# Kernel optimization log

Hardware: AMD Instinct MI355X
Metric: run time of the kernel (lower is better)

The kernel has to match this reference:

```python
import jax, jax.numpy as jnp
import numpy as np
from jax import lax

DN = ('NHWC', 'HWIO', 'NHWC')
EPS = 1e-3  # keras BatchNormalization default epsilon


def conv2d(x, w):
    return lax.conv_general_dilated(x, w, (1, 1), 'SAME', dimension_numbers=DN)


def convlstm2d(x, W, U, b):
    # x: (B,T,H,Wd,Cin); W: (kh,kw,Cin,4F); U: (kh,kw,F,4F); b: (4F,)
    # Keras ConvLSTM2D, gate order i,f,c,o; recurrent_activation=sigmoid, activation=relu
    B, T, H, Wd, _ = x.shape
    F = U.shape[2]
    xz = conv2d(x.reshape(B * T, H, Wd, -1), W).reshape(B, T, H, Wd, 4 * F) + b

    def step(carry, xt):
        h, c = carry
        z = xt + conv2d(h, U)
        i, f, g, o = jnp.split(z, 4, axis=-1)
        i = jax.nn.sigmoid(i)
        f = jax.nn.sigmoid(f)
        c = f * c + i * jax.nn.relu(g)
        h = jax.nn.sigmoid(o) * jax.nn.relu(c)
        return (h, c), h

    h0 = jnp.zeros((B, H, Wd, F), x.dtype)
    _, hs = lax.scan(step, (h0, h0), jnp.moveaxis(xz, 0, 1))  # (T,B,H,W,F)
    return jnp.moveaxis(hs, 0, 1)


def batchnorm(x, gamma, beta, mean, var):
    return (x - mean) * (gamma * lax.rsqrt(var + EPS)) + beta


def maxpool_122(x):
    # MaxPooling3D pool=(1,2,2), strides=(1,2,2), padding='same', channels_last
    return lax.reduce_window(x, -jnp.inf, lax.max, (1, 1, 2, 2, 1), (1, 1, 2, 2, 1), 'SAME')


def setup_inputs() -> dict:
    key = jax.random.key(0)
    ks = iter(jax.random.split(key, 32))
    s = 0.05
    d = {
        'x': jax.random.normal(next(ks), (8, 10, 64, 64, 3), jnp.float32),
        'W1': jax.random.normal(next(ks), (5, 5, 3, 128), jnp.float32) * s,
        'U1': jax.random.normal(next(ks), (5, 5, 32, 128), jnp.float32) * s,
        'b1': jnp.zeros((128,), jnp.float32),
        'g1': jax.random.uniform(next(ks), (32,), jnp.float32, 0.5, 1.5),
        'be1': jax.random.normal(next(ks), (32,), jnp.float32) * 0.1,
        'm1': jax.random.normal(next(ks), (32,), jnp.float32) * 0.1,
        'v1': jax.random.uniform(next(ks), (32,), jnp.float32, 0.5, 1.5),
        'W2': jax.random.normal(next(ks), (5, 5, 32, 128), jnp.float32) * s,
        'U2': jax.random.normal(next(ks), (5, 5, 32, 128), jnp.float32) * s,
        'b2': jnp.zeros((128,), jnp.float32),
        'g2': jax.random.uniform(next(ks), (32,), jnp.float32, 0.5, 1.5),
        'be2': jax.random.normal(next(ks), (32,), jnp.float32) * 0.1,
        'm2': jax.random.normal(next(ks), (32,), jnp.float32) * 0.1,
        'v2': jax.random.uniform(next(ks), (32,), jnp.float32, 0.5, 1.5),
        'W3': jax.random.normal(next(ks), (3, 3, 32, 128), jnp.float32) * s,
        'U3': jax.random.normal(next(ks), (3, 3, 32, 128), jnp.float32) * s,
        'b3': jnp.zeros((128,), jnp.float32),
        'g3': jax.random.uniform(next(ks), (32,), jnp.float32, 0.5, 1.5),
        'be3': jax.random.normal(next(ks), (32,), jnp.float32) * 0.1,
        'm3': jax.random.normal(next(ks), (32,), jnp.float32) * 0.1,
        'v3': jax.random.uniform(next(ks), (32,), jnp.float32, 0.5, 1.5),
        'Wd1': jax.random.normal(next(ks), (20480, 64), jnp.float32) * 0.01,
        'bd1': jnp.zeros((64,), jnp.float32),
        'Wd2': jax.random.normal(next(ks), (64, 10), jnp.float32) * 0.1,
        'bd2': jnp.zeros((10,), jnp.float32),
    }
    return d


def reference(x, W1, U1, b1, g1, be1, m1, v1, W2, U2, b2, g2, be2, m2, v2,
              W3, U3, b3, g3, be3, m3, v3, Wd1, bd1, Wd2, bd2):
    x = convlstm2d(x, W1, U1, b1)
    x = maxpool_122(batchnorm(x, g1, be1, m1, v1))
    x = convlstm2d(x, W2, U2, b2)
    x = maxpool_122(batchnorm(x, g2, be2, m2, v2))
    x = convlstm2d(x, W3, U3, b3)
    x = maxpool_122(batchnorm(x, g3, be3, m3, v3))
    x = x.reshape(x.shape[0], -1)  # (B, T*H*W*F) = (8, 20480)
    x = jax.nn.softmax(x @ Wd1 + bd1, axis=-1)
    return jax.nn.softmax(x @ Wd2 + bd2, axis=-1)
```

## Files before the change

### kernel.cpp

```cpp
#include <hip/hip_runtime.h>

using short8 = __attribute__((ext_vector_type(8))) short;
using f32x4  = __attribute__((ext_vector_type(4))) float;

__device__ __forceinline__ unsigned short f2bf(float x){
    unsigned u = __float_as_uint(x);
    unsigned r = (u + 0x7FFFu + ((u>>16)&1u)) >> 16;
    return (unsigned short)r;
}
__device__ __forceinline__ float bf2f(unsigned short h){
    return __uint_as_float(((unsigned)h)<<16);
}
__device__ __forceinline__ float sigf(float x){ return 1.0f/(1.0f+__expf(-x)); }
__device__ __forceinline__ int swz(int b){ return b ^ (((b>>7)&7)<<4); }

struct SP {
    const float *x;
    const float *g1,*be1,*m1,*v1;
    const float *g2,*be2,*m2,*v2;
    const float *g3,*be3,*m3,*v3;
    unsigned short *hs1,*hs2,*hs3;
    unsigned short *pl1,*pl2,*pl3;
    float *cst1,*cst2,*cst3;
    const short8 *U1b,*W1b,*U2b,*W2b,*U3b,*W3b;
    const float *bp;
    unsigned *ctr;
};

__global__ __launch_bounds__(256)
void xform_all(const float* __restrict__ U1, const float* __restrict__ W1,
               const float* __restrict__ U2, const float* __restrict__ W2,
               const float* __restrict__ U3, const float* __restrict__ W3,
               const float* __restrict__ b1, const float* __restrict__ b2, const float* __restrict__ b3,
               short8* __restrict__ U1b, short8* __restrict__ W1b,
               short8* __restrict__ U2b, short8* __restrict__ W2b,
               short8* __restrict__ U3b, short8* __restrict__ W3b,
               float* __restrict__ bp)
{
    int i = blockIdx.x*256 + threadIdx.x;
    if (i >= 49536) return;
    if (i >= 49152) {
        int j = i - 49152, layer = j >> 7, np = j & 127;
        int oc = ((np>>4)&3)*32 + (np>>6)*16 + (np&15);
        const float* bs = layer==0 ? b1 : (layer==1 ? b2 : b3);
        bp[j] = bs[oc];
        return;
    }
    const float* src; short8* dst; int base, kmax;
    if      (i < 12800){ src=U1; dst=U1b; base=0;     kmax=800; }
    else if (i < 14336){ src=W1; dst=W1b; base=12800; kmax=75;  }
    else if (i < 27136){ src=U2; dst=U2b; base=14336; kmax=800; }
    else if (i < 39936){ src=W2; dst=W2b; base=27136; kmax=800; }
    else if (i < 44544){ src=U3; dst=U3b; base=39936; kmax=288; }
    else               { src=W3; dst=W3b; base=44544; kmax=288; }
    int j = i - base;
    int lane = j & 63, nt = (j >> 6) & 7, tap = j >> 9;
    int np = nt*16 + (lane & 15);
    int oc = ((np>>4)&3)*32 + (np>>6)*16 + (np&15);
    int g = lane >> 4;
    short8 pk;
    #pragma unroll
    for (int e = 0; e < 8; ++e) {
        int k = tap*32 + g*8 + e;
        unsigned short v = (k < kmax) ? f2bf(src[(long)k*128 + oc]) : (unsigned short)0;
        pk[e] = (short)v;
    }
    dst[j] = pk;
}

template<int K, int PW, int MT2>
__device__ __forceinline__ void conv_taps(f32x4 (&acc)[MT2][4],
    const unsigned short* patch, const short8* Wf, int mh, int nh, int l15, int g4, int lane)
{
    constexpr int NTAP = K*K;
    const short8* ub = Wf + nh*4*64 + lane;
    short8 bA0 = ub[0], bA1 = ub[64], bA2 = ub[128], bA3 = ub[192];
    short8 bB0 = bA0, bB1 = bA1, bB2 = bA2, bB3 = bA3;
    { const short8* u = ub + 512; bB0=u[0]; bB1=u[64]; bB2=u[128]; bB3=u[192]; }
    #pragma unroll 1
    for (int tp = 0; tp < NTAP; tp += 2) {
        {
            int dy = tp / K, dx = tp % K;
            #pragma unroll
            for (int mt = 0; mt < MT2; ++mt) {
                short8 af = *(const short8*)((const char*)patch +
                    swz(((mh*MT2 + mt + dy)*PW + l15 + dx)*64 + g4*16));
                acc[mt][0] = __builtin_amdgcn_mfma_f32_16x16x32_bf16(af, bA0, acc[mt][0], 0,0,0);
                acc[mt][1] = __builtin_amdgcn_mfma_f32_16x16x32_bf16(af, bA1, acc[mt][1], 0,0,0);
                acc[mt][2] = __builtin_amdgcn_mfma_f32_16x16x32_bf16(af, bA2, acc[mt][2], 0,0,0);
                acc[mt][3] = __builtin_amdgcn_mfma_f32_16x16x32_bf16(af, bA3, acc[mt][3], 0,0,0);
            }
            if (tp + 2 < NTAP) { const short8* u = ub + (long)(tp+2)*512; bA0=u[0];bA1=u[64];bA2=u[128];bA3=u[192]; }
        }
        if (tp + 1 < NTAP) {
            int dy = (tp+1) / K, dx = (tp+1) % K;
            #pragma unroll
            for (int mt = 0; mt < MT2; ++mt) {
                short8 af = *(const short8*)((const char*)patch +
                    swz(((mh*MT2 + mt + dy)*PW + l15 + dx)*64 + g4*16));
                acc[mt][0] = __builtin_amdgcn_mfma_f32_16x16x32_bf16(af, bB0, acc[mt][0], 0,0,0);
                acc[mt][1] = __builtin_amdgcn_mfma_f32_16x16x32_bf16(af, bB1, acc[mt][1], 0,0,0);
                acc[mt][2] = __builtin_amdgcn_mfma_f32_16x16x32_bf16(af, bB2, acc[mt][2], 0,0,0);
                acc[mt][3] = __builtin_amdgcn_mfma_f32_16x16x32_bf16(af, bB3, acc[mt][3], 0,0,0);
            }
            if (tp + 3 < NTAP) { const short8* u = ub + (long)(tp+3)*512; bB0=u[0];bB1=u[64];bB2=u[128];bB3=u[192]; }
        }
    }
}

template<int MT2>
__device__ __forceinline__ void lstm_epilogue(
    f32x4 (&acc)[MT2][4], unsigned short* hs, float* cst, unsigned short* plout,
    const float* gg, const float* bb, const float* mm, const float* vv,
    int H, int W, int n, int y0, int x0, int t, int mh, int nh, int l15, int g4, int first)
{
    const int f = nh*16 + l15;
    const int xt = x0 >> 4;
    const float sc = gg[f] * rsqrtf(vv[f] + 1e-3f);
    const float sh = bb[f] - mm[f]*sc;
    unsigned short* outh = hs + ((long)n*10 + t)*(long)H*W*32;
    float hv[MT2][4];
    #pragma unroll
    for (int mt = 0; mt < MT2; ++mt) {
        int row = y0 + mh*MT2 + mt;
        long tb = ((long)(n*H + row)*(W>>4) + xt)*512 + f*16 + g4*4;
        f32x4 cold = first ? (f32x4){0.f,0.f,0.f,0.f} : *(const f32x4*)&cst[tb];
        f32x4 cn;
        #pragma unroll
        for (int j = 0; j < 4; ++j) {
            float zi = acc[mt][0][j];
            float zf = acc[mt][1][j];
            float zg = acc[mt][2][j];
            float zo = acc[mt][3][j];
            float c2 = sigf(zf)*cold[j] + sigf(zi)*fmaxf(zg, 0.0f);
            cn[j] = c2;
            float h = sigf(zo)*fmaxf(c2, 0.0f);
            hv[mt][j] = h;
            outh[((long)row*W + (x0 + g4*4 + j))*32 + f] = f2bf(h);
        }
        *(f32x4*)&cst[tb] = cn;
    }
    #pragma unroll
    for (int mp = 0; mp < MT2/2; ++mp) {
        int orow = (y0>>1) + mh*(MT2/2) + mp;
        #pragma unroll
        for (int jp = 0; jp < 2; ++jp) {
            int ocol = (x0>>1) + g4*2 + jp;
            float mx = fmaxf(fmaxf(hv[2*mp][2*jp],   hv[2*mp][2*jp+1]),
                             fmaxf(hv[2*mp+1][2*jp], hv[2*mp+1][2*jp+1]));
            plout[(((long)(n*10 + t)*(H>>1) + orow)*(W>>1) + ocol)*32 + f] = f2bf(mx*sc + sh);
        }
    }
}

__device__ void l1_step(char* smem, const SP& p, int n, int y0, int x0, int t)
{
    constexpr int PAD = 2, PH = 12, PW = 20, MT2 = 4, MPX = 128;
    const int H = 64, W = 64;
    unsigned short* patch_s = (unsigned short*)smem;
    unsigned short* xpk_s   = (unsigned short*)(smem + 15360);
    unsigned short* xraw    = (unsigned short*)(smem + 39936);
    const int tid = threadIdx.x;
    const int lane = tid & 63, wid = tid >> 6;
    const int mh = wid >> 1, nh = wid & 1;
    const int l15 = lane & 15, g4 = lane >> 4;
    const int first = (t == 0);

    short8 z8 = {0,0,0,0,0,0,0,0};
    #pragma unroll
    for (int c = tid; c < MPX*96/8; c += 256)
        ((short8*)xpk_s)[c] = z8;

    if (tid < PH*PW) {
        const float* xs = p.x + ((long)n*10 + t)*4096*3;
        int gy = y0 - PAD + tid / PW;
        int gx = x0 - PAD + tid % PW;
        float v0=0.f, v1=0.f, v2=0.f;
        if ((unsigned)gy < 64u && (unsigned)gx < 64u) {
            const float* b = xs + ((long)gy*64 + gx)*3;
            v0 = b[0]; v1 = b[1]; v2 = b[2];
        }
        xraw[tid*3]   = f2bf(v0);
        xraw[tid*3+1] = f2bf(v1);
        xraw[tid*3+2] = f2bf(v2);
    }

    if (!first) {
        const unsigned short* s = p.hs1 + ((long)n*10 + (t-1))*(long)H*W*32;
        #pragma unroll 1
        for (int c = tid; c < PH*PW*4; c += 256) {
            int pix = c >> 2, gq = c & 3;
            int pr = pix / PW, pc = pix % PW;
            int gy = y0 - PAD + pr, gx = x0 - PAD + pc;
            short8 v = z8;
            if ((unsigned)gy < 64u && (unsigned)gx < 64u)
                v = *(const short8*)(s + ((long)gy*W + gx)*32 + gq*8);
            *(short8*)((char*)patch_s + swz(pix*64 + gq*16)) = v;
        }
    }
    __syncthreads();

    #pragma unroll 1
    for (int c = tid; c < MPX*25; c += 256) {
        int px = c & (MPX-1), tap = c >> 7;
        int dy = (tap*52) >> 8, dx = tap - dy*5;
        int pi = ((px>>4) + dy)*PW + (px&15) + dx;
        int o = px*192 + tap*6;
        *(unsigned short*)((char*)xpk_s + swz(o))   = xraw[pi*3];
        *(unsigned short*)((char*)xpk_s + swz(o+2)) = xraw[pi*3+1];
        *(unsigned short*)((char*)xpk_s + swz(o+4)) = xraw[pi*3+2];
    }
    __syncthreads();

    f32x4 acc[MT2][4];
    #pragma unroll
    for (int ntl = 0; ntl < 4; ++ntl) {
        float bv = p.bp[(nh*4+ntl)*16 + l15];
        #pragma unroll
        for (int mt = 0; mt < MT2; ++mt)
            acc[mt][ntl] = (f32x4){bv,bv,bv,bv};
    }
    #pragma unroll 1
    for (int c = 0; c < 3; ++c) {
        const short8* wp = p.W1b + ((long)c*8 + nh*4)*64 + lane;
        short8 bf0 = wp[0], bf1 = wp[64], bf2 = wp[128], bf3 = wp[192];
        #pragma unroll
        for (int mt = 0; mt < MT2; ++mt) {
            short8 af = *(const short8*)((const char*)xpk_s +
                swz(((mh*MT2+mt)*16 + l15)*192 + c*64 + g4*16));
            acc[mt][0] = __builtin_amdgcn_mfma_f32_16x16x32_bf16(af, bf0, acc[mt][0], 0,0,0);
            acc[mt][1] = __builtin_amdgcn_mfma_f32_16x16x32_bf16(af, bf1, acc[mt][1], 0,0,0);
            acc[mt][2] = __builtin_amdgcn_mfma_f32_16x16x32_bf16(af, bf2, acc[mt][2], 0,0,0);
            acc[mt][3] = __builtin_amdgcn_mfma_f32_16x16x32_bf16(af, bf3, acc[mt][3], 0,0,0);
        }
    }
    if (!first)
        conv_taps<5,PW,MT2>(acc, patch_s, p.U1b, mh, nh, l15, g4, lane);

    lstm_epilogue<MT2>(acc, p.hs1, p.cst1, p.pl1, p.g1, p.be1, p.m1, p.v1,
                       H, W, n, y0, x0, t, mh, nh, l15, g4, first);
}

template<int K, int HH>
__device__ void l23_step(char* smem, const SP& p,
    unsigned short* hs, const unsigned short* plin, unsigned short* plout, float* cst,
    const short8* Ufr, const short8* Wfr, const float* bp,
    const float* gg, const float* bb, const float* mm, const float* vv,
    int n, int y0, int x0, int t)
{
    constexpr int TH = 4, PAD = K/2, PH = TH+K-1, PW = 16+K-1, MT2 = 2;
    const int H = HH, W = HH;
    unsigned short* patchH = (unsigned short*)smem;
    unsigned short* patchX = (unsigned short*)(smem + PH*PW*64);

    const int tid = threadIdx.x;
    const int lane = tid & 63, wid = tid >> 6;
    const int mh = wid >> 1, nh = wid & 1;
    const int l15 = lane & 15, g4 = lane >> 4;
    const int first = (t == 0);

    const unsigned short* hsrc = hs + ((long)n*10 + (t-1))*(long)H*W*32;
    const unsigned short* xsrc = plin + ((long)n*10 + t)*(long)H*W*32;
    short8 z8 = {0,0,0,0,0,0,0,0};
    #pragma unroll 1
    for (int c = tid; c < PH*PW*4; c += 256) {
        int pix = c >> 2, gq = c & 3;
        int pr = pix / PW, pc = pix % PW;
        int gy = y0 - PAD + pr, gx = x0 - PAD + pc;
        short8 vx = z8, vh = z8;
        if ((unsigned)gy < (unsigned)H && (unsigned)gx < (unsigned)W) {
            vx = *(const short8*)(xsrc + ((long)gy*W + gx)*32 + gq*8);
            if (!first) vh = *(const short8*)(hsrc + ((long)gy*W + gx)*32 + gq*8);
        }
        *(short8*)((char*)patchX + swz(pix*64 + gq*16)) = vx;
        *(short8*)((char*)patchH + swz(pix*64 + gq*16)) = vh;
    }
    __syncthreads();

    f32x4 acc[MT2][4];
    #pragma unroll
    for (int ntl = 0; ntl < 4; ++ntl) {
        float bv = bp[(nh*4+ntl)*16 + l15];
        #pragma unroll
        for (int mt = 0; mt < MT2; ++mt)
            acc[mt][ntl] = (f32x4){bv,bv,bv,bv};
    }
    conv_taps<K,PW,MT2>(acc, patchX, Wfr, mh, nh, l15, g4, lane);
    if (!first) conv_taps<K,PW,MT2>(acc, patchH, Ufr, mh, nh, l15, g4, lane);

    lstm_epilogue<MT2>(acc, hs, cst, plout, gg, bb, mm, vv,
                       H, W, n, y0, x0, t, mh, nh, l15, g4, first);
}

__global__ __launch_bounds__(256)
void stage_k(SP p, int s)
{
    __shared__ __align__(16) char smem[41472];
    const int bid = blockIdx.x;
    if (bid < 256) {
        int t = s;
        if (t < 10) {
            int n = bid >> 5, rem = bid & 31;
            l1_step(smem, p, n, (rem >> 2)*8, (rem & 3)*16, t);
        }
    } else if (bid < 384) {
        int t = s - 1;
        if (t >= 0 && t < 10) {
            int idx = bid - 256;
            int n = idx >> 4, rem = idx & 15;
            l23_step<5,32>(smem, p, p.hs2, p.pl1, p.pl2, p.cst2,
                           p.U2b, p.W2b, p.bp + 128,
                           p.g2, p.be2, p.m2, p.v2,
                           n, (rem >> 1)*4, (rem & 1)*16, t);
        } else if (s == 0 && bid == 256 && threadIdx.x == 0) {
            __hip_atomic_store(p.ctr, 0u, __ATOMIC_RELEASE, __HIP_MEMORY_SCOPE_AGENT);
        }
    } else {
        int t = s - 2;
        if (t >= 0 && t < 10) {
            int idx = bid - 384;
            int n = idx >> 2, rem = idx & 3;
            l23_step<3,16>(smem, p, p.hs3, p.pl2, p.pl3, p.cst3,
                           p.U3b, p.W3b, p.bp + 256,
                           p.g3, p.be3, p.m3, p.v3,
                           n, rem*4, 0, t);
        }
    }
}

__global__ __launch_bounds__(256)
void dense_all(const unsigned short* __restrict__ flat, const float* __restrict__ Wd1,
               const float* __restrict__ bd1, const float* __restrict__ Wd2,
               const float* __restrict__ bd2, float* __restrict__ partial,
               unsigned* __restrict__ ctr, float* __restrict__ outp)
{
    __shared__ __align__(16) float xs[2048];
    __shared__ unsigned rank_s;
    const int kc = blockIdx.x, k0 = kc*256;
    const int t = threadIdx.x;
    {
        int r = t >> 5, kb = (t & 31)*8;
        short8 v = *(const short8*)(flat + (long)r*20480 + k0 + kb);
        #pragma unroll
        for (int e = 0; e < 8; ++e) xs[(kb+e)*8 + r] = bf2f((unsigned short)v[e]);
    }
    __syncthreads();
    const int c = t & 63, seg = t >> 6;
    f32x4 accA = {0,0,0,0}, accB = {0,0,0,0};
    #pragma unroll 4
    for (int kk = seg*64; kk < seg*64 + 64; ++kk) {
        float w = Wd1[(long)(k0+kk)*64 + c];
        f32x4 xa = *(const f32x4*)&xs[kk*8];
        f32x4 xb = *(const f32x4*)&xs[kk*8 + 4];
        #pragma unroll
        for (int j = 0; j < 4; ++j) { accA[j] = fmaf(xa[j], w, accA[j]); accB[j] = fmaf(xb[j], w, accB[j]); }
    }
    __syncthreads();
    #pragma unroll
    for (int j = 0; j < 4; ++j) {
        xs[(seg*8 + j)*64 + c]     = accA[j];
        xs[(seg*8 + 4 + j)*64 + c] = accB[j];
    }
    __syncthreads();
    #pragma unroll
    for (int o = t; o < 512; o += 256) {
        int r = o >> 6, cc = o & 63;
        partial[(long)kc*512 + o] = (xs[(0*8+r)*64+cc] + xs[(1*8+r)*64+cc])
                                  + (xs[(2*8+r)*64+cc] + xs[(3*8+r)*64+cc]);
    }
    __syncthreads();
    if (t == 0) {
        __builtin_amdgcn_fence(__ATOMIC_RELEASE, "agent");
        rank_s = __hip_atomic_fetch_add(ctr, 1u, __ATOMIC_ACQ_REL, __HIP_MEMORY_SCOPE_AGENT);
    }
    __syncthreads();
    if (rank_s != 79) return;
    __builtin_amdgcn_fence(__ATOMIC_ACQUIRE, "agent");

    float* d1  = xs;
    float* l2s = xs + 512;
    #pragma unroll
    for (int rr = 0; rr < 2; ++rr) {
        int idx = rr*256 + t;
        int cc = idx & 63;
        float s = bd1[cc];
        #pragma unroll 4
        for (int q = 0; q < 80; ++q) s += partial[q*512 + idx];
        float mx = s;
        for (int o = 32; o > 0; o >>= 1) mx = fmaxf(mx, __shfl_xor(mx, o, 64));
        float e = __expf(s - mx);
        float sm = e;
        for (int o = 32; o > 0; o >>= 1) sm += __shfl_xor(sm, o, 64);
        d1[idx] = e / sm;
    }
    __syncthreads();
    if (t < 80) {
        int r = t / 10, o = t % 10;
        float l = bd2[o];
        #pragma unroll 8
        for (int cc = 0; cc < 64; ++cc) l = fmaf(d1[r*64 + cc], Wd2[cc*10 + o], l);
        l2s[t] = l;
    }
    __syncthreads();
    if (t < 8) {
        float mx2 = l2s[t*10];
        #pragma unroll
        for (int j = 1; j < 10; ++j) mx2 = fmaxf(mx2, l2s[t*10 + j]);
        float ev[10], s2 = 0.f;
        #pragma unroll
        for (int j = 0; j < 10; ++j) { ev[j] = __expf(l2s[t*10 + j] - mx2); s2 += ev[j]; }
        #pragma unroll
        for (int j = 0; j < 10; ++j) outp[t*10 + j] = ev[j] / s2;
    }
}

extern "C" void kernel_launch(void* const* d_in, const int* in_sizes, int n_in,
                              void* d_out, int out_size, void* d_ws, size_t ws_size,
                              hipStream_t stream)
{
    const float* Wd1 = (const float*)d_in[22];
    const float* bd1 = (const float*)d_in[23];
    const float* Wd2 = (const float*)d_in[24];
    const float* bd2 = (const float*)d_in[25];

    char* ws = (char*)d_ws;
    SP p;
    p.x   = (const float*)d_in[0];
    p.g1  = (const float*)d_in[4];  p.be1 = (const float*)d_in[5];  p.m1 = (const float*)d_in[6];  p.v1 = (const float*)d_in[7];
    p.g2  = (const float*)d_in[11]; p.be2 = (const float*)d_in[12]; p.m2 = (const float*)d_in[13]; p.v2 = (const float*)d_in[14];
    p.g3  = (const float*)d_in[18]; p.be3 = (const float*)d_in[19]; p.m3 = (const float*)d_in[20]; p.v3 = (const float*)d_in[21];

    p.hs1 = (unsigned short*)(ws);
    p.hs2 = (unsigned short*)(ws + 20971520);
    p.hs3 = (unsigned short*)(ws + 26214400);
    p.cst1 = (float*)(ws + 27525120);
    p.cst2 = (float*)(ws + 31719424);
    p.cst3 = (float*)(ws + 32768000);
    p.pl1 = (unsigned short*)(ws + 33030144);
    p.pl2 = (unsigned short*)(ws + 38273024);
    p.pl3 = (unsigned short*)(ws + 39583744);
    short8* U1b = (short8*)(ws + 39911424);
    short8* W1b = (short8*)(ws + 40116224);
    short8* U2b = (short8*)(ws + 40140800);
    short8* W2b = (short8*)(ws + 40345600);
    short8* U3b = (short8*)(ws + 40550400);
    short8* W3b = (short8*)(ws + 40624128);
    float*  bp  = (float*)(ws + 40697856);
    float*  partial = (float*)(ws + 40699392);
    p.ctr = (unsigned*)(ws + 40863232);
    p.U1b = U1b; p.W1b = W1b; p.U2b = U2b; p.W2b = W2b; p.U3b = U3b; p.W3b = W3b;
    p.bp = bp;

    xform_all<<<194, 256, 0, stream>>>(
        (const float*)d_in[2], (const float*)d_in[1],
        (const float*)d_in[9], (const float*)d_in[8],
        (const float*)d_in[16], (const float*)d_in[15],
        (const float*)d_in[3], (const float*)d_in[10], (const float*)d_in[17],
        U1b, W1b, U2b, W2b, U3b, W3b, bp);

    for (int s = 0; s < 12; ++s)
        stage_k<<<416, 256, 0, stream>>>(p, s);

    dense_all<<<80, 256, 0, stream>>>(p.pl3, Wd1, bd1, Wd2, bd2, partial,
                                      p.ctr, (float*)d_out);
}
```

Before: 224.6 us.

## Precompute layer-1 input convolution one step ahead in extra wavefront blocks

```diff
diff --git a/kernel.cpp b/kernel.cpp
--- a/kernel.cpp
+++ b/kernel.cpp
@@ -1,7 +1,8 @@
 #include <hip/hip_runtime.h>
 
-using short8 = __attribute__((ext_vector_type(8))) short;
-using f32x4  = __attribute__((ext_vector_type(4))) float;
+using short8  = __attribute__((ext_vector_type(8))) short;
+using short4v = __attribute__((ext_vector_type(4))) short;
+using f32x4   = __attribute__((ext_vector_type(4))) float;
 
 __device__ __forceinline__ unsigned short f2bf(float x){
     unsigned u = __float_as_uint(x);
@@ -22,6 +23,7 @@
     unsigned short *hs1,*hs2,*hs3;
     unsigned short *pl1,*pl2,*pl3;
     float *cst1,*cst2,*cst3;
+    unsigned short *xzp;
     const short8 *U1b,*W1b,*U2b,*W2b,*U3b,*W3b;
     const float *bp;
     unsigned *ctr;
@@ -153,6 +155,86 @@
     }
 }
 
+__device__ void xz_step(char* smem, const SP& p, int n, int y0, int x0, int t)
+{
+    constexpr int PAD = 2, PH = 12, PW = 20, MT2 = 4, MPX = 128;
+    unsigned short* xpk_s = (unsigned short*)(smem + 15360);
+    unsigned short* xraw  = (unsigned short*)(smem + 39936);
+    const int tid = threadIdx.x;
+    const int lane = tid & 63, wid = tid >> 6;
+    const int mh = wid >> 1, nh = wid & 1;
+    const int l15 = lane & 15, g4 = lane >> 4;
+    const int xt = x0 >> 4;
+
+    short8 z8 = {0,0,0,0,0,0,0,0};
+    #pragma unroll
+    for (int c = tid; c < MPX*96/8; c += 256)
+        ((short8*)xpk_s)[c] = z8;
+
+    if (tid < PH*PW) {
+        const float* xs = p.x + ((long)n*10 + t)*4096*3;
+        int gy = y0 - PAD + tid / PW;
+        int gx = x0 - PAD + tid % PW;
+        float v0=0.f, v1=0.f, v2=0.f;
+        if ((unsigned)gy < 64u && (unsigned)gx < 64u) {
+            const float* b = xs + ((long)gy*64 + gx)*3;
+            v0 = b[0]; v1 = b[1]; v2 = b[2];
+        }
+        xraw[tid*3]   = f2bf(v0);
+        xraw[tid*3+1] = f2bf(v1);
+        xraw[tid*3+2] = f2bf(v2);
+    }
+    __syncthreads();
+    #pragma unroll 1
+    for (int c = tid; c < MPX*25; c += 256) {
+        int px = c & (MPX-1), tap = c >> 7;
+        int dy = (tap*52) >> 8, dx = tap - dy*5;
+        int pi = ((px>>4) + dy)*PW + (px&15) + dx;
+        int o = px*192 + tap*6;
+        *(unsigned short*)((char*)xpk_s + swz(o))   = xraw[pi*3];
+        *(unsigned short*)((char*)xpk_s + swz(o+2)) = xraw[pi*3+1];
+        *(unsigned short*)((char*)xpk_s + swz(o+4)) = xraw[pi*3+2];
+    }
+    __syncthreads();
+
+    f32x4 acc[MT2][4];
+    #pragma unroll
+    for (int ntl = 0; ntl < 4; ++ntl) {
+        float bv = p.bp[(nh*4+ntl)*16 + l15];
+        #pragma unroll
+        for (int mt = 0; mt < MT2; ++mt)
+            acc[mt][ntl] = (f32x4){bv,bv,bv,bv};
+    }
+    #pragma unroll 1
+    for (int c = 0; c < 3; ++c) {
+        const short8* wp = p.W1b + ((long)c*8 + nh*4)*64 + lane;
+        short8 bf0 = wp[0], bf1 = wp[64], bf2 = wp[128], bf3 = wp[192];
+        #pragma unroll
+        for (int mt = 0; mt < MT2; ++mt) {
+            short8 af = *(const short8*)((const char*)xpk_s +
+                swz(((mh*MT2+mt)*16 + l15)*192 + c*64 + g4*16));
+            acc[mt][0] = __builtin_amdgcn_mfma_f32_16x16x32_bf16(af, bf0, acc[mt][0], 0,0,0);
+            acc[mt][1] = __builtin_amdgcn_mfma_f32_16x16x32_bf16(af, bf1, acc[mt][1], 0,0,0);
+            acc[mt][2] = __builtin_amdgcn_mfma_f32_16x16x32_bf16(af, bf2, acc[mt][2], 0,0,0);
+            acc[mt][3] = __builtin_amdgcn_mfma_f32_16x16x32_bf16(af, bf3, acc[mt][3], 0,0,0);
+        }
+    }
+    unsigned short* xzb = p.xzp + (size_t)(t & 1)*4194304;
+    #pragma unroll
+    for (int mt = 0; mt < MT2; ++mt) {
+        int row = y0 + mh*MT2 + mt;
+        long base = (((long)(n*64 + row))*4 + xt)*2048;
+        #pragma unroll
+        for (int ntl = 0; ntl < 4; ++ntl) {
+            int np = (nh*4+ntl)*16 + l15;
+            short4v s;
+            #pragma unroll
+            for (int j = 0; j < 4; ++j) s[j] = (short)f2bf(acc[mt][ntl][j]);
+            *(short4v*)&xzb[base + np*16 + g4*4] = s;
+        }
+    }
+}
+
 __device__ void l1_step(char* smem, const SP& p, int n, int y0, int x0, int t)
 {
     constexpr int PAD = 2, PH = 12, PW = 20, MT2 = 4, MPX = 128;
@@ -165,27 +247,39 @@
     const int mh = wid >> 1, nh = wid & 1;
     const int l15 = lane & 15, g4 = lane >> 4;
     const int first = (t == 0);
-
+    const int xt = x0 >> 4;
     short8 z8 = {0,0,0,0,0,0,0,0};
-    #pragma unroll
-    for (int c = tid; c < MPX*96/8; c += 256)
-        ((short8*)xpk_s)[c] = z8;
-
-    if (tid < PH*PW) {
-        const float* xs = p.x + ((long)n*10 + t)*4096*3;
-        int gy = y0 - PAD + tid / PW;
-        int gx = x0 - PAD + tid % PW;
-        float v0=0.f, v1=0.f, v2=0.f;
-        if ((unsigned)gy < 64u && (unsigned)gx < 64u) {
-            const float* b = xs + ((long)gy*64 + gx)*3;
-            v0 = b[0]; v1 = b[1]; v2 = b[2];
-        }
-        xraw[tid*3]   = f2bf(v0);
-        xraw[tid*3+1] = f2bf(v1);
-        xraw[tid*3+2] = f2bf(v2);
-    }
-
-    if (!first) {
+
+    if (first) {
+        #pragma unroll
+        for (int c = tid; c < MPX*96/8; c += 256)
+            ((short8*)xpk_s)[c] = z8;
+        if (tid < PH*PW) {
+            const float* xs = p.x + ((long)n*10 + t)*4096*3;
+            int gy = y0 - PAD + tid / PW;
+            int gx = x0 - PAD + tid % PW;
+            float v0=0.f, v1=0.f, v2=0.f;
+            if ((unsigned)gy < 64u && (unsigned)gx < 64u) {
+                const float* b = xs + ((long)gy*64 + gx)*3;
+                v0 = b[0]; v1 = b[1]; v2 = b[2];
+            }
+            xraw[tid*3]   = f2bf(v0);
+            xraw[tid*3+1] = f2bf(v1);
+            xraw[tid*3+2] = f2bf(v2);
+        }
+        __syncthreads();
+        #pragma unroll 1
+        for (int c = tid; c < MPX*25; c += 256) {
+            int px = c & (MPX-1), tap = c >> 7;
+            int dy = (tap*52) >> 8, dx = tap - dy*5;
+            int pi = ((px>>4) + dy)*PW + (px&15) + dx;
+            int o = px*192 + tap*6;
+            *(unsigned short*)((char*)xpk_s + swz(o))   = xraw[pi*3];
+            *(unsigned short*)((char*)xpk_s + swz(o+2)) = xraw[pi*3+1];
+            *(unsigned short*)((char*)xpk_s + swz(o+4)) = xraw[pi*3+2];
+        }
+        __syncthreads();
+    } else {
         const unsigned short* s = p.hs1 + ((long)n*10 + (t-1))*(long)H*W*32;
         #pragma unroll 1
         for (int c = tid; c < PH*PW*4; c += 256) {
@@ -197,45 +291,48 @@
                 v = *(const short8*)(s + ((long)gy*W + gx)*32 + gq*8);
             *(short8*)((char*)patch_s + swz(pix*64 + gq*16)) = v;
         }
-    }
-    __syncthreads();
-
-    #pragma unroll 1
-    for (int c = tid; c < MPX*25; c += 256) {
-        int px = c & (MPX-1), tap = c >> 7;
-        int dy = (tap*52) >> 8, dx = tap - dy*5;
-        int pi = ((px>>4) + dy)*PW + (px&15) + dx;
-        int o = px*192 + tap*6;
-        *(unsigned short*)((char*)xpk_s + swz(o))   = xraw[pi*3];
-        *(unsigned short*)((char*)xpk_s + swz(o+2)) = xraw[pi*3+1];
-        *(unsigned short*)((char*)xpk_s + swz(o+4)) = xraw[pi*3+2];
-    }
-    __syncthreads();
+        __syncthreads();
+    }
 
     f32x4 acc[MT2][4];
-    #pragma unroll
-    for (int ntl = 0; ntl < 4; ++ntl) {
-        float bv = p.bp[(nh*4+ntl)*16 + l15];
-        #pragma unroll
-        for (int mt = 0; mt < MT2; ++mt)
-            acc[mt][ntl] = (f32x4){bv,bv,bv,bv};
-    }
-    #pragma unroll 1
-    for (int c = 0; c < 3; ++c) {
-        const short8* wp = p.W1b + ((long)c*8 + nh*4)*64 + lane;
-        short8 bf0 = wp[0], bf1 = wp[64], bf2 = wp[128], bf3 = wp[192];
+    if (first) {
+        #pragma unroll
+        for (int ntl = 0; ntl < 4; ++ntl) {
+            float bv = p.bp[(nh*4+ntl)*16 + l15];
+            #pragma unroll
+            for (int mt = 0; mt < MT2; ++mt)
+                acc[mt][ntl] = (f32x4){bv,bv,bv,bv};
+        }
+        #pragma unroll 1
+        for (int c = 0; c < 3; ++c) {
+            const short8* wp = p.W1b + ((long)c*8 + nh*4)*64 + lane;
+            short8 bf0 = wp[0], bf1 = wp[64], bf2 = wp[128], bf3 = wp[192];
+            #pragma unroll
+            for (int mt = 0; mt < MT2; ++mt) {
+                short8 af = *(const short8*)((const char*)xpk_s +
+                    swz(((mh*MT2+mt)*16 + l15)*192 + c*64 + g4*16));
+                acc[mt][0] = __builtin_amdgcn_mfma_f32_16x16x32_bf16(af, bf0, acc[mt][0], 0,0,0);
+                acc[mt][1] = __builtin_amdgcn_mfma_f32_16x16x32_bf16(af, bf1, acc[mt][1], 0,0,0);
+                acc[mt][2] = __builtin_amdgcn_mfma_f32_16x16x32_bf16(af, bf2, acc[mt][2], 0,0,0);
+                acc[mt][3] = __builtin_amdgcn_mfma_f32_16x16x32_bf16(af, bf3, acc[mt][3], 0,0,0);
+            }
+        }
+    } else {
+        const unsigned short* xzb = p.xzp + (size_t)(t & 1)*4194304;
         #pragma unroll
         for (int mt = 0; mt < MT2; ++mt) {
-            short8 af = *(const short8*)((const char*)xpk_s +
-                swz(((mh*MT2+mt)*16 + l15)*192 + c*64 + g4*16));
-            acc[mt][0] = __builtin_amdgcn_mfma_f32_16x16x32_bf16(af, bf0, acc[mt][0], 0,0,0);
-            acc[mt][1] = __builtin_amdgcn_mfma_f32_16x16x32_bf16(af, bf1, acc[mt][1], 0,0,0);
-            acc[mt][2] = __builtin_amdgcn_mfma_f32_16x16x32_bf16(af, bf2, acc[mt][2], 0,0,0);
-            acc[mt][3] = __builtin_amdgcn_mfma_f32_16x16x32_bf16(af, bf3, acc[mt][3], 0,0,0);
-        }
-    }
-    if (!first)
+            int row = y0 + mh*MT2 + mt;
+            long base = (((long)(n*64 + row))*4 + xt)*2048;
+            #pragma unroll
+            for (int ntl = 0; ntl < 4; ++ntl) {
+                int np = (nh*4+ntl)*16 + l15;
+                short4v v = *(const short4v*)&xzb[base + np*16 + g4*4];
+                acc[mt][ntl] = (f32x4){bf2f((unsigned short)v[0]), bf2f((unsigned short)v[1]),
+                                       bf2f((unsigned short)v[2]), bf2f((unsigned short)v[3])};
+            }
+        }
         conv_taps<5,PW,MT2>(acc, patch_s, p.U1b, mh, nh, l15, g4, lane);
+    }
 
     lstm_epilogue<MT2>(acc, p.hs1, p.cst1, p.pl1, p.g1, p.be1, p.m1, p.v1,
                        H, W, n, y0, x0, t, mh, nh, l15, g4, first);
@@ -315,7 +412,7 @@
         } else if (s == 0 && bid == 256 && threadIdx.x == 0) {
             __hip_atomic_store(p.ctr, 0u, __ATOMIC_RELEASE, __HIP_MEMORY_SCOPE_AGENT);
         }
-    } else {
+    } else if (bid < 416) {
         int t = s - 2;
         if (t >= 0 && t < 10) {
             int idx = bid - 384;
@@ -324,6 +421,13 @@
                            p.U3b, p.W3b, p.bp + 256,
                            p.g3, p.be3, p.m3, p.v3,
                            n, rem*4, 0, t);
+        }
+    } else {
+        int t = s + 1;
+        if (t >= 1 && t < 10) {
+            int idx = bid - 416;
+            int n = idx >> 5, rem = idx & 31;
+            xz_step(smem, p, n, (rem >> 2)*8, (rem & 3)*16, t);
         }
     }
 }
@@ -448,6 +552,7 @@
     float*  bp  = (float*)(ws + 40697856);
     float*  partial = (float*)(ws + 40699392);
     p.ctr = (unsigned*)(ws + 40863232);
+    p.xzp = (unsigned short*)(ws + 40863296);
     p.U1b = U1b; p.W1b = W1b; p.U2b = U2b; p.W2b = W2b; p.U3b = U3b; p.W3b = W3b;
     p.bp = bp;
 
@@ -459,7 +564,7 @@
         U1b, W1b, U2b, W2b, U3b, W3b, bp);
 
     for (int s = 0; s < 12; ++s)
-        stage_k<<<416, 256, 0, stream>>>(p, s);
+        stage_k<<<672, 256, 0, stream>>>(p, s);
 
     dense_all<<<80, 256, 0, stream>>>(p.pl3, Wd1, bd1, Wd2, bd2, partial,
                                       p.ctr, (float*)d_out);
```

New measurement: 261.3 us. 1.16x slower.
